# Kernel tuning notes

Measured on AMD Instinct MI355X. Metric: run time of the kernel, lower is better.

Reference implementation:

```python
import jax, jax.numpy as jnp
import numpy as np

B, L, HIDDEN, HEAD_DIM = 8, 1024, 1024, 64


def setup_inputs() -> dict:
    key = jax.random.key(0)
    ks = jax.random.split(key, 11)
    s = 1.0 / np.sqrt(HIDDEN)
    return {
        "query": jax.random.normal(ks[0], (B, L, HIDDEN), jnp.float32),
        "key": jax.random.normal(ks[1], (B, L, HIDDEN), jnp.float32),
        "value": jax.random.normal(ks[2], (B, L, HIDDEN), jnp.float32),
        "k_bias_matrix": jax.random.normal(ks[3], (L, L, HEAD_DIM), jnp.float32) * 0.02,
        "v_bias_matrix": jax.random.normal(ks[4], (L, L, HEAD_DIM), jnp.float32) * 0.02,
        "Wq": jax.random.normal(ks[5], (HIDDEN, HEAD_DIM), jnp.float32) * s,
        "bq": jnp.zeros((HEAD_DIM,), jnp.float32),
        "Wk": jax.random.normal(ks[6], (HIDDEN, HEAD_DIM), jnp.float32) * s,
        "bk": jnp.zeros((HEAD_DIM,), jnp.float32),
        "Wv": jax.random.normal(ks[7], (HIDDEN, HEAD_DIM), jnp.float32) * s,
        "bv": jnp.zeros((HEAD_DIM,), jnp.float32),
        "mask": jnp.ones((B, L), jnp.int32),
    }


def reference(query, key, value, k_bias_matrix, v_bias_matrix, Wq, bq, Wk, bk, Wv, bv, mask):
    # projections to head_dim
    q = query @ Wq + bq  # [B,L,D]
    k = key @ Wk + bk    # [B,L,D]
    v = value @ Wv + bv  # [B,L,D]
    # content scores + relative key-bias scores (Shaw et al.)
    attn_1 = jnp.einsum('bqd,bkd->bqk', q, k)              # [B,L,L]
    attn_2 = jnp.einsum('bqd,qkd->bqk', q, k_bias_matrix)  # [B,L,L]
    scores = (attn_1 + attn_2) / jnp.sqrt(jnp.asarray(q.shape[-1], q.dtype))
    scores = jnp.where(mask[:, None, :] == 0, jnp.asarray(-1e9, scores.dtype), scores)
    w = jax.nn.softmax(scores, axis=-1)                    # [B,L,L]
    values_1 = jnp.einsum('bqk,bkd->bqd', w, v)
    values_2 = jnp.einsum('bqk,qkd->bqd', w, v_bias_matrix)
    return values_1 + values_2
```

## Files before the change

kernel.cpp:

```cpp
#include <hip/hip_runtime.h>

#define B_ 8
#define L_ 1024
#define HID_ 1024
#define D_ 64

typedef short bf16x8 __attribute__((ext_vector_type(8)));
typedef float f32x4 __attribute__((ext_vector_type(4)));

__device__ inline short f2bf(float f) {
    unsigned u = __builtin_bit_cast(unsigned, f);
    unsigned r = (u + 0x7fffu + ((u >> 16) & 1u)) >> 16;
    return (short)r;
}

__global__ __launch_bounds__(256) void proj_kernel(
    const float* __restrict__ query, const float* __restrict__ key, const float* __restrict__ value,
    const float* __restrict__ Wq, const float* __restrict__ bq,
    const float* __restrict__ Wk, const float* __restrict__ bk,
    const float* __restrict__ Wv, const float* __restrict__ bv,
    float* __restrict__ qp, float* __restrict__ kp, float* __restrict__ vp)
{
    const int which = blockIdx.y;
    const float* in   = which == 0 ? query : (which == 1 ? key : value);
    const float* W    = which == 0 ? Wq : (which == 1 ? Wk : Wv);
    const float* bias = which == 0 ? bq : (which == 1 ? bk : bv);
    float* out        = which == 0 ? qp : (which == 1 ? kp : vp);

    __shared__ float Xs[64][68];
    __shared__ float Ws[64][64];

    const int t  = threadIdx.x;
    const int tx = t & 15;
    const int ty = t >> 4;
    const int r0 = blockIdx.x * 64;

    float acc[4][4] = {};
    for (int kk = 0; kk < HID_; kk += 64) {
        {
            const int r  = t >> 4;
            const int c4 = t & 15;
            #pragma unroll
            for (int i = 0; i < 4; i++) {
                float4 x = *(const float4*)(in + (size_t)(r0 + r + 16 * i) * HID_ + kk + 4 * c4);
                *(float4*)(&Xs[r + 16 * i][4 * c4]) = x;
                float4 w = *(const float4*)(W + (size_t)(kk + r + 16 * i) * D_ + 4 * c4);
                *(float4*)(&Ws[r + 16 * i][4 * c4]) = w;
            }
        }
        __syncthreads();
        #pragma unroll 8
        for (int k = 0; k < 64; k++) {
            float4 b4 = *(const float4*)(&Ws[k][4 * tx]);
            #pragma unroll
            for (int i = 0; i < 4; i++) {
                float a = Xs[4 * ty + i][k];
                acc[i][0] += a * b4.x;
                acc[i][1] += a * b4.y;
                acc[i][2] += a * b4.z;
                acc[i][3] += a * b4.w;
            }
        }
        __syncthreads();
    }
    float4 bb = *(const float4*)(bias + 4 * tx);
    #pragma unroll
    for (int i = 0; i < 4; i++) {
        float4 o;
        o.x = acc[i][0] + bb.x; o.y = acc[i][1] + bb.y;
        o.z = acc[i][2] + bb.z; o.w = acc[i][3] + bb.w;
        *(float4*)(out + (size_t)(r0 + 4 * ty + i) * D_ + 4 * tx) = o;
    }
}

__global__ __launch_bounds__(256) void attn1_kernel(
    const float* __restrict__ qp, const float* __restrict__ kp,
    const int* __restrict__ mask, float* __restrict__ s1)
{
    const int b  = blockIdx.z;
    const int q0 = blockIdx.y * 128;
    const int k0 = blockIdx.x * 128;
    __shared__ float qs[128][68];
    __shared__ float ks[128][68];
    const int t = threadIdx.x;
    {
        const int row = t >> 4;
        const int c4  = t & 15;
        #pragma unroll
        for (int i = 0; i < 8; i++) {
            int r = row + 16 * i;
            *(float4*)&qs[r][c4 * 4] = *(const float4*)(qp + ((size_t)b * L_ + q0 + r) * D_ + c4 * 4);
            *(float4*)&ks[r][c4 * 4] = *(const float4*)(kp + ((size_t)b * L_ + k0 + r) * D_ + c4 * 4);
        }
    }
    __syncthreads();
    const int tx = t & 15, ty = t >> 4;
    float acc[8][8] = {};
    for (int d4 = 0; d4 < 16; d4++) {
        float4 qv[8], kv[8];
        #pragma unroll
        for (int i = 0; i < 8; i++) qv[i] = *(const float4*)&qs[ty + 16 * i][d4 * 4];
        #pragma unroll
        for (int j = 0; j < 8; j++) kv[j] = *(const float4*)&ks[tx + 16 * j][d4 * 4];
        #pragma unroll
        for (int i = 0; i < 8; i++)
            #pragma unroll
            for (int j = 0; j < 8; j++)
                acc[i][j] += qv[i].x * kv[j].x + qv[i].y * kv[j].y +
                             qv[i].z * kv[j].z + qv[i].w * kv[j].w;
    }
    #pragma unroll
    for (int j = 0; j < 8; j++) {
        int kg = k0 + tx + 16 * j;
        bool live = mask[b * L_ + kg] != 0;
        #pragma unroll
        for (int i = 0; i < 8; i++) {
            int qg = q0 + ty + 16 * i;
            s1[((size_t)b * L_ + qg) * L_ + kg] = live ? acc[i][j] * 0.125f : -1e9f;
        }
    }
}

#define KS_ 1032
__global__ __launch_bounds__(512) void row_kernel(
    const float* __restrict__ qp, const float* __restrict__ vp,
    const float* __restrict__ kb, const float* __restrict__ vb,
    const float* __restrict__ s1, float* __restrict__ out)
{
    __shared__ float sc[2 * 8 * KS_];
    __shared__ short qbf[2 * 16 * 64];
    const int t = threadIdx.x;
    const int wave = t >> 6, lane = t & 63;
    const int q0 = blockIdx.x * 2;

    #pragma unroll
    for (int i = 0; i < 4; i++) {
        int idx = t + 512 * i;
        int d = idx & 63, bq = idx >> 6;
        int b = bq & 15, q = bq >> 4;
        float v = (b < 8) ? 0.125f * qp[((size_t)b * L_ + q0 + q) * D_ + d] : 0.0f;
        qbf[idx] = f2bf(v);
    }
    __syncthreads();

    for (int job = wave; job < 128; job += 8) {
        int q = job >> 6, kt = job & 63;
        int k0 = kt * 16;
        const float* abase = kb + ((size_t)(q0 + q) * L_ + k0 + (lane & 15)) * D_ + (lane >> 4) * 8;
        f32x4 acc = {0.f, 0.f, 0.f, 0.f};
        #pragma unroll
        for (int h = 0; h < 2; h++) {
            float4 x0 = *(const float4*)(abase + h * 32);
            float4 x1 = *(const float4*)(abase + h * 32 + 4);
            bf16x8 a;
            a[0] = f2bf(x0.x); a[1] = f2bf(x0.y); a[2] = f2bf(x0.z); a[3] = f2bf(x0.w);
            a[4] = f2bf(x1.x); a[5] = f2bf(x1.y); a[6] = f2bf(x1.z); a[7] = f2bf(x1.w);
            bf16x8 bq = *(const bf16x8*)&qbf[(q * 16 + (lane & 15)) * 64 + h * 32 + (lane >> 4) * 8];
            acc = __builtin_amdgcn_mfma_f32_16x16x32_bf16(a, bq, acc, 0, 0, 0);
        }
        int b = lane & 15;
        if (b < 8) {
            float* dst = &sc[(q * 8 + b) * KS_ + k0 + (lane >> 4) * 4];
            dst[0] = acc[0]; dst[1] = acc[1]; dst[2] = acc[2]; dst[3] = acc[3];
        }
    }
    __syncthreads();

    #pragma unroll
    for (int i = 0; i < 8; i++) {
        int idx = t + 512 * i;
        int c4 = idx & 255;
        int row = idx >> 8;
        int b = row & 7, q = row >> 3;
        float4 s = *(const float4*)(s1 + ((size_t)b * L_ + q0 + q) * L_ + c4 * 4);
        float* dst = &sc[(q * 8 + b) * KS_ + c4 * 4];
        float4 cur = *(float4*)dst;
        cur.x += s.x; cur.y += s.y; cur.z += s.z; cur.w += s.w;
        *(float4*)dst = cur;
    }
    __syncthreads();

    for (int r = wave; r < 16; r += 8) {
        float* rowp = &sc[r * KS_];
        float4 x[4];
        float m = -1e30f;
        #pragma unroll
        for (int j = 0; j < 4; j++) {
            x[j] = *(const float4*)&rowp[lane * 4 + 256 * j];
            m = fmaxf(m, fmaxf(fmaxf(x[j].x, x[j].y), fmaxf(x[j].z, x[j].w)));
        }
        #pragma unroll
        for (int off = 32; off; off >>= 1) m = fmaxf(m, __shfl_xor(m, off));
        float s = 0.f;
        #pragma unroll
        for (int j = 0; j < 4; j++) {
            x[j].x = __expf(x[j].x - m); x[j].y = __expf(x[j].y - m);
            x[j].z = __expf(x[j].z - m); x[j].w = __expf(x[j].w - m);
            s += x[j].x + x[j].y + x[j].z + x[j].w;
        }
        #pragma unroll
        for (int off = 32; off; off >>= 1) s += __shfl_xor(s, off);
        float inv = 1.0f / s;
        #pragma unroll
        for (int j = 0; j < 4; j++) {
            x[j].x *= inv; x[j].y *= inv; x[j].z *= inv; x[j].w *= inv;
            *(float4*)&rowp[lane * 4 + 256 * j] = x[j];
        }
    }
    __syncthreads();

    {
        const int q  = wave >> 2;
        const int kq = (wave & 3) * 256;
        const int kl = lane >> 4;
        const int d4 = lane & 15;
        float acc[8][4] = {};
        const float* vbbase = vb + ((size_t)(q0 + q) * L_ + kq + kl) * D_ + d4 * 4;
        #pragma unroll 2
        for (int j = 0; j < 64; j++) {
            int k = kq + j * 4 + kl;
            float4 vb4 = *(const float4*)(vbbase + (size_t)j * 4 * D_);
            #pragma unroll
            for (int b = 0; b < 8; b++) {
                float4 vp4 = *(const float4*)(vp + ((size_t)b * L_ + k) * D_ + d4 * 4);
                float wgt = sc[(q * 8 + b) * KS_ + k];
                acc[b][0] += wgt * (vb4.x + vp4.x);
                acc[b][1] += wgt * (vb4.y + vp4.y);
                acc[b][2] += wgt * (vb4.z + vp4.z);
                acc[b][3] += wgt * (vb4.w + vp4.w);
            }
        }
        #pragma unroll
        for (int b = 0; b < 8; b++)
            #pragma unroll
            for (int j = 0; j < 4; j++) {
                float v = acc[b][j];
                v += __shfl_down(v, 32);
                v += __shfl_down(v, 16);
                acc[b][j] = v;
            }
        if (lane < 16) {
            #pragma unroll
            for (int b = 0; b < 8; b++)
                #pragma unroll
                for (int j = 0; j < 4; j++)
                    atomicAdd(out + ((size_t)b * L_ + q0 + q) * D_ + d4 * 4 + j, acc[b][j]);
        }
    }
}

extern "C" void kernel_launch(void* const* d_in, const int* in_sizes, int n_in,
                              void* d_out, int out_size, void* d_ws, size_t ws_size,
                              hipStream_t stream)
{
    const float* query = (const float*)d_in[0];
    const float* key   = (const float*)d_in[1];
    const float* value = (const float*)d_in[2];
    const float* kb    = (const float*)d_in[3];
    const float* vb    = (const float*)d_in[4];
    const float* Wq    = (const float*)d_in[5];
    const float* bq    = (const float*)d_in[6];
    const float* Wk    = (const float*)d_in[7];
    const float* bk    = (const float*)d_in[8];
    const float* Wv    = (const float*)d_in[9];
    const float* bv    = (const float*)d_in[10];
    const int*   mask  = (const int*)d_in[11];
    float* out = (float*)d_out;

    float* ws = (float*)d_ws;
    const size_t PROJ = (size_t)B_ * L_ * D_;
    float* qp = ws;
    float* kp = ws + PROJ;
    float* vp = ws + 2 * PROJ;
    float* s1 = ws + 3 * PROJ;

    hipMemsetAsync(d_out, 0, (size_t)B_ * L_ * D_ * sizeof(float), stream);
    proj_kernel<<<dim3(128, 3), 256, 0, stream>>>(query, key, value,
                                                  Wq, bq, Wk, bk, Wv, bv,
                                                  qp, kp, vp);
    attn1_kernel<<<dim3(8, 8, 8), 256, 0, stream>>>(qp, kp, mask, s1);
    row_kernel<<<512, 512, 0, stream>>>(qp, vp, kb, vb, s1, out);
}
```

Before: 713.0 us.

## Split w@v into separate tiled kernel, drop atomics via shared-memory reduction

```diff
diff --git a/kernel.cpp b/kernel.cpp
--- a/kernel.cpp
+++ b/kernel.cpp
@@ -123,9 +123,9 @@
 
 #define KS_ 1032
 __global__ __launch_bounds__(512) void row_kernel(
-    const float* __restrict__ qp, const float* __restrict__ vp,
-    const float* __restrict__ kb, const float* __restrict__ vb,
-    const float* __restrict__ s1, float* __restrict__ out)
+    const float* __restrict__ qp, const float* __restrict__ kb,
+    const float* __restrict__ vb, float* __restrict__ s1w,
+    float* __restrict__ out)
 {
     __shared__ float sc[2 * 8 * KS_];
     __shared__ short qbf[2 * 16 * 64];
@@ -172,7 +172,7 @@
         int c4 = idx & 255;
         int row = idx >> 8;
         int b = row & 7, q = row >> 3;
-        float4 s = *(const float4*)(s1 + ((size_t)b * L_ + q0 + q) * L_ + c4 * 4);
+        float4 s = *(const float4*)(s1w + ((size_t)b * L_ + q0 + q) * L_ + c4 * 4);
         float* dst = &sc[(q * 8 + b) * KS_ + c4 * 4];
         float4 cur = *(float4*)dst;
         cur.x += s.x; cur.y += s.y; cur.z += s.z; cur.w += s.w;
@@ -181,7 +181,9 @@
     __syncthreads();
 
     for (int r = wave; r < 16; r += 8) {
+        int q = r >> 3, b = r & 7;
         float* rowp = &sc[r * KS_];
+        float* wrow = s1w + ((size_t)b * L_ + q0 + q) * L_;
         float4 x[4];
         float m = -1e30f;
         #pragma unroll
@@ -205,29 +207,30 @@
         for (int j = 0; j < 4; j++) {
             x[j].x *= inv; x[j].y *= inv; x[j].z *= inv; x[j].w *= inv;
             *(float4*)&rowp[lane * 4 + 256 * j] = x[j];
+            *(float4*)&wrow[lane * 4 + 256 * j] = x[j];
         }
     }
     __syncthreads();
 
     {
         const int q  = wave >> 2;
-        const int kq = (wave & 3) * 256;
+        const int kqi = wave & 3;
+        const int kq = kqi * 256;
         const int kl = lane >> 4;
         const int d4 = lane & 15;
         float acc[8][4] = {};
         const float* vbbase = vb + ((size_t)(q0 + q) * L_ + kq + kl) * D_ + d4 * 4;
-        #pragma unroll 2
+        #pragma unroll 4
         for (int j = 0; j < 64; j++) {
             int k = kq + j * 4 + kl;
             float4 vb4 = *(const float4*)(vbbase + (size_t)j * 4 * D_);
             #pragma unroll
             for (int b = 0; b < 8; b++) {
-                float4 vp4 = *(const float4*)(vp + ((size_t)b * L_ + k) * D_ + d4 * 4);
                 float wgt = sc[(q * 8 + b) * KS_ + k];
-                acc[b][0] += wgt * (vb4.x + vp4.x);
-                acc[b][1] += wgt * (vb4.y + vp4.y);
-                acc[b][2] += wgt * (vb4.z + vp4.z);
-                acc[b][3] += wgt * (vb4.w + vp4.w);
+                acc[b][0] += wgt * vb4.x;
+                acc[b][1] += wgt * vb4.y;
+                acc[b][2] += wgt * vb4.z;
+                acc[b][3] += wgt * vb4.w;
             }
         }
         #pragma unroll
@@ -239,13 +242,71 @@
                 v += __shfl_down(v, 16);
                 acc[b][j] = v;
             }
+        __syncthreads();
+        float* part = sc;
         if (lane < 16) {
             #pragma unroll
-            for (int b = 0; b < 8; b++)
-                #pragma unroll
-                for (int j = 0; j < 4; j++)
-                    atomicAdd(out + ((size_t)b * L_ + q0 + q) * D_ + d4 * 4 + j, acc[b][j]);
-        }
+            for (int b = 0; b < 8; b++) {
+                float4 o; o.x = acc[b][0]; o.y = acc[b][1]; o.z = acc[b][2]; o.w = acc[b][3];
+                *(float4*)&part[(((q * 4 + kqi) * 8) + b) * 64 + d4 * 4] = o;
+            }
+        }
+        __syncthreads();
+        for (int i = t; i < 1024; i += 512) {
+            int d = i & 63; int bq = i >> 6; int b = bq & 7; int q2 = bq >> 3;
+            float s = part[((q2 * 4 + 0) * 8 + b) * 64 + d] +
+                      part[((q2 * 4 + 1) * 8 + b) * 64 + d] +
+                      part[((q2 * 4 + 2) * 8 + b) * 64 + d] +
+                      part[((q2 * 4 + 3) * 8 + b) * 64 + d];
+            out[((size_t)b * L_ + q0 + q2) * D_ + d] = s;
+        }
+    }
+}
+
+__global__ __launch_bounds__(256) void pv_kernel(
+    const float* __restrict__ w, const float* __restrict__ vp, float* __restrict__ out)
+{
+    const int b  = blockIdx.y;
+    const int q0 = blockIdx.x * 32;
+    __shared__ float ws_[32][68];
+    __shared__ float vs[64][64];
+    const int t  = threadIdx.x;
+    const int tx = t & 15;
+    const int ty = t >> 4;
+    float acc[2][4] = {};
+    for (int kk = 0; kk < L_; kk += 64) {
+        #pragma unroll
+        for (int i = 0; i < 2; i++) {
+            int f4 = t + 256 * i;
+            int qi = f4 >> 4, kc = f4 & 15;
+            float4 x = *(const float4*)(w + ((size_t)b * L_ + q0 + qi) * L_ + kk + 4 * kc);
+            *(float4*)(&ws_[qi][4 * kc]) = x;
+        }
+        #pragma unroll
+        for (int i = 0; i < 4; i++) {
+            int f4 = t + 256 * i;
+            int kr = f4 >> 4, dc = f4 & 15;
+            float4 x = *(const float4*)(vp + ((size_t)b * L_ + kk + kr) * D_ + 4 * dc);
+            *(float4*)(&vs[kr][4 * dc]) = x;
+        }
+        __syncthreads();
+        #pragma unroll 8
+        for (int k = 0; k < 64; k++) {
+            float4 v4 = *(const float4*)(&vs[k][4 * tx]);
+            float a0 = ws_[2 * ty][k], a1 = ws_[2 * ty + 1][k];
+            acc[0][0] += a0 * v4.x; acc[0][1] += a0 * v4.y;
+            acc[0][2] += a0 * v4.z; acc[0][3] += a0 * v4.w;
+            acc[1][0] += a1 * v4.x; acc[1][1] += a1 * v4.y;
+            acc[1][2] += a1 * v4.z; acc[1][3] += a1 * v4.w;
+        }
+        __syncthreads();
+    }
+    #pragma unroll
+    for (int i = 0; i < 2; i++) {
+        float* dst = out + ((size_t)b * L_ + q0 + 2 * ty + i) * D_ + 4 * tx;
+        float4 o = *(const float4*)dst;
+        o.x += acc[i][0]; o.y += acc[i][1]; o.z += acc[i][2]; o.w += acc[i][3];
+        *(float4*)dst = o;
     }
 }
 
@@ -274,10 +335,10 @@
     float* vp = ws + 2 * PROJ;
     float* s1 = ws + 3 * PROJ;
 
-    hipMemsetAsync(d_out, 0, (size_t)B_ * L_ * D_ * sizeof(float), stream);
     proj_kernel<<<dim3(128, 3), 256, 0, stream>>>(query, key, value,
                                                   Wq, bq, Wk, bk, Wv, bv,
                                                   qp, kp, vp);
     attn1_kernel<<<dim3(8, 8, 8), 256, 0, stream>>>(qp, kp, mask, s1);
-    row_kernel<<<512, 512, 0, stream>>>(qp, vp, kb, vb, s1, out);
-}
+    row_kernel<<<512, 512, 0, stream>>>(qp, kb, vb, s1, out);
+    pv_kernel<<<dim3(32, 8), 256, 0, stream>>>(s1, vp, out);
+}
```

Measured after the change: 691.4 us. 3.0% less time.
